# Kernel tuning notes

Hardware: AMD Instinct MI355X
Metric: run time of the kernel (lower is better)

The kernel has to match this reference:

```python
import jax, jax.numpy as jnp
import numpy as np

K = 3  # kernel_size
PAD = 1


def _unfold3x3(x):
    # x: [b, c, h, w] -> patches [b, c, k*k, h, w] matching torch.nn.Unfold
    # ordering (row-major over the kernel window, channel outermost).
    b, c, h, w = x.shape
    xp = jnp.pad(x, ((0, 0), (0, 0), (PAD, PAD), (PAD, PAD)))
    patches = jnp.stack(
        [xp[:, :, i:i + h, j:j + w] for i in range(K) for j in range(K)],
        axis=2,
    )
    return patches  # [b, c, 9, h, w]


def setup_inputs() -> dict:
    key = jax.random.key(0)
    k1, k2, k3, k4 = jax.random.split(key, 4)
    b, c, h, w = 8, 64, 128, 128
    out_ch = 64
    x = jax.random.normal(k1, (b, c, h, w), dtype=jnp.float32)
    guide_ch = jax.random.normal(k2, (b, c, h, w), dtype=jnp.float32)
    guide_sp = jax.random.normal(k3, (b, K * K, h, w), dtype=jnp.float32)
    # kaiming_normal_ fan_out on [out, in, k^2, 1, 1]: fan_out = out * k^2 * 1 * 1?
    # torch fan_out for 5D conv weight = out_channels * receptive_field (k^2*1*1)
    fan_out = out_ch * (K * K)
    std = np.sqrt(2.0 / fan_out)
    weight = jax.random.normal(k4, (out_ch, c, K * K), dtype=jnp.float32) * std
    return {"x": x, "guide_ch": guide_ch, "guide_sp": guide_sp, "weight": weight}


def reference(x, guide_ch, guide_sp, weight):
    # filter: [b, c, k^2, h, w] = 1 + tanh(guide_ch[:, :, None] + guide_sp[:, None])
    filt = 1.0 + jnp.tanh(guide_ch[:, :, None, :, :] + guide_sp[:, None, :, :, :])
    patches = _unfold3x3(x)  # [b, c, 9, h, w]
    # conv3d with weight [out, in, k^2, 1, 1] == per-pixel reduction over (c, k^2)
    out = jnp.einsum('bckhw,ock->bohw', patches * filt, weight)
    return out
```

## Files before the change

### kernel.cpp

```cpp
#include <hip/hip_runtime.h>
#include <hip/hip_bf16.h>

typedef short short8 __attribute__((ext_vector_type(8)));
typedef float floatx4 __attribute__((ext_vector_type(4)));
typedef unsigned uintx4 __attribute__((ext_vector_type(4)));

#define HWSZ 16384
#define WD 128
#define CD 64
#define OD 64
#define XSTR 72
#define OSTR 136
#define L2E2 2.8853900817779268f

__device__ __forceinline__ short f2bf(float f) {
    unsigned u = __builtin_bit_cast(unsigned, f);
    u += 0x7FFFu + ((u >> 16) & 1u);
    return (short)(u >> 16);
}

__device__ __forceinline__ unsigned pack2bf(float a, float b) {
    __hip_bfloat162 h = __float22bfloat162_rn(float2{a, b});
    unsigned u;
    __builtin_memcpy(&u, &h, 4);
    return u;
}

__device__ __forceinline__ float bf2f(short s) {
    return __builtin_bit_cast(float, ((unsigned)(unsigned short)s) << 16);
}

__global__ void prepack_w(const float* __restrict__ wgt, unsigned short* __restrict__ wp) {
    int idx = blockIdx.x * 256 + threadIdx.x;
    if (idx < 9 * 64 * 64) {
        int k = idx >> 12, o = (idx >> 6) & 63, c = idx & 63;
        wp[idx] = (unsigned short)f2bf(2.0f * wgt[o * 576 + c * 9 + k]);
    }
}

__global__ __launch_bounds__(256, 3)
void paka_kernel(const float* __restrict__ x, const float* __restrict__ gc,
                 const float* __restrict__ gs, const float* __restrict__ wgt,
                 const unsigned short* __restrict__ wp, float* __restrict__ out)
{
    __shared__ union {
        short xl[130 * XSTR];
        float o[64 * OSTR];
    } lds;

    const int tid  = threadIdx.x;
    const int wave = tid >> 6;
    const int lane = tid & 63;

    const int id  = blockIdx.x;
    const int swz = (id & 7) * 128 + (id >> 3);
    const int b = swz >> 7;
    const int h = swz & 127;

    const float* xb  = x  + (size_t)b * CD * HWSZ;
    const float* gcb = gc + (size_t)b * CD * HWSZ;
    const float* gsb = gs + (size_t)b * 9 * HWSZ;

    const int row = lane & 15;
    const int q   = lane >> 4;
    const int mt0 = wave * 2;

    float eg[2][2][8];
    #pragma unroll
    for (int mt = 0; mt < 2; ++mt) {
        int p = (mt0 + mt) * 16 + row;
        #pragma unroll
        for (int ks = 0; ks < 2; ++ks)
            #pragma unroll
            for (int j = 0; j < 8; ++j) {
                int c = ks * 32 + q * 8 + j;
                eg[mt][ks][j] = __builtin_amdgcn_exp2f(gcb[(size_t)c * HWSZ + h * WD + p] * L2E2);
            }
    }
    float esv[9][2];
    #pragma unroll
    for (int k = 0; k < 9; ++k)
        #pragma unroll
        for (int mt = 0; mt < 2; ++mt) {
            int p = (mt0 + mt) * 16 + row;
            esv[k][mt] = __builtin_amdgcn_exp2f(gsb[k * HWSZ + h * WD + p] * L2E2);
        }

    if (tid < 32)
        *(unsigned*)&lds.xl[0 * XSTR + tid * 2] = 0u;
    else if (tid < 64)
        *(unsigned*)&lds.xl[129 * XSTR + (tid - 32) * 2] = 0u;

    floatx4 acc[2][4];
    #pragma unroll
    for (int i = 0; i < 2; ++i)
        #pragma unroll
        for (int n = 0; n < 4; ++n)
            acc[i][n] = (floatx4){0.f, 0.f, 0.f, 0.f};

    #pragma unroll
    for (int dh = 0; dh < 3; ++dh) {
        const int hh = h + dh - 1;
        if ((unsigned)hh >= 128u) continue;

        __syncthreads();

        {
            const int g = tid >> 5;
            const float* xg = xb + (size_t)(8 * g) * HWSZ + hh * WD;
            #pragma unroll
            for (int it = 0; it < 4; ++it) {
                int p = it * 32 + (tid & 31);
                uintx4 pv;
                #pragma unroll
                for (int cc = 0; cc < 4; ++cc) {
                    float a  = xg[(size_t)(2 * cc) * HWSZ + p];
                    float b2 = xg[(size_t)(2 * cc + 1) * HWSZ + p];
                    pv[cc] = pack2bf(a, b2);
                }
                *(uintx4*)&lds.xl[(p + 1) * XSTR + g * 8] = pv;
            }
        }

        __syncthreads();

        #pragma unroll
        for (int dw = 0; dw < 3; ++dw) {
            const int k = dh * 3 + dw;
            #pragma unroll
            for (int ks = 0; ks < 2; ++ks) {
                short8 bv0, bv1, bv2, bv3;
                if (wp) {
                    const unsigned short* wk = wp + k * 4096 + ks * 32 + q * 8;
                    bv0 = *(const short8*)&wk[(0 * 16 + row) * 64];
                    bv1 = *(const short8*)&wk[(1 * 16 + row) * 64];
                    bv2 = *(const short8*)&wk[(2 * 16 + row) * 64];
                    bv3 = *(const short8*)&wk[(3 * 16 + row) * 64];
                } else {
                    #pragma unroll
                    for (int j = 0; j < 8; ++j) {
                        int c = ks * 32 + q * 8 + j;
                        bv0[j] = f2bf(2.0f * wgt[(0*16+row) * 576 + c * 9 + k]);
                        bv1[j] = f2bf(2.0f * wgt[(1*16+row) * 576 + c * 9 + k]);
                        bv2[j] = f2bf(2.0f * wgt[(2*16+row) * 576 + c * 9 + k]);
                        bv3[j] = f2bf(2.0f * wgt[(3*16+row) * 576 + c * 9 + k]);
                    }
                }

                short8 af[2];
                #pragma unroll
                for (int mt = 0; mt < 2; ++mt) {
                    int wslot = (mt0 + mt) * 16 + row + dw;
                    short8 raw = *(const short8*)&lds.xl[wslot * XSTR + ks * 32 + q * 8];
                    float es = esv[k][mt];
                    #pragma unroll
                    for (int jj = 0; jj < 4; ++jj) {
                        float d0 = fmaf(eg[mt][ks][2 * jj],     es, 1.0f);
                        float d1 = fmaf(eg[mt][ks][2 * jj + 1], es, 1.0f);
                        float r0 = __builtin_amdgcn_rcpf(d0);
                        float r1 = __builtin_amdgcn_rcpf(d1);
                        float x0 = bf2f(raw[2 * jj]);
                        float x1 = bf2f(raw[2 * jj + 1]);
                        float t0 = fmaf(-x0, r0, x0);
                        float t1 = fmaf(-x1, r1, x1);
                        ((unsigned*)&af[mt])[jj] = pack2bf(t0, t1);
                    }
                }
                acc[0][0] = __builtin_amdgcn_mfma_f32_16x16x32_bf16(af[0], bv0, acc[0][0], 0, 0, 0);
                acc[1][0] = __builtin_amdgcn_mfma_f32_16x16x32_bf16(af[1], bv0, acc[1][0], 0, 0, 0);
                acc[0][1] = __builtin_amdgcn_mfma_f32_16x16x32_bf16(af[0], bv1, acc[0][1], 0, 0, 0);
                acc[1][1] = __builtin_amdgcn_mfma_f32_16x16x32_bf16(af[1], bv1, acc[1][1], 0, 0, 0);
                acc[0][2] = __builtin_amdgcn_mfma_f32_16x16x32_bf16(af[0], bv2, acc[0][2], 0, 0, 0);
                acc[1][2] = __builtin_amdgcn_mfma_f32_16x16x32_bf16(af[1], bv2, acc[1][2], 0, 0, 0);
                acc[0][3] = __builtin_amdgcn_mfma_f32_16x16x32_bf16(af[0], bv3, acc[0][3], 0, 0, 0);
                acc[1][3] = __builtin_amdgcn_mfma_f32_16x16x32_bf16(af[1], bv3, acc[1][3], 0, 0, 0);
            }
        }
    }

    __syncthreads();

    #pragma unroll
    for (int i = 0; i < 2; ++i) {
        int prow = (mt0 + i) * 16 + q * 4;
        #pragma unroll
        for (int nt = 0; nt < 4; ++nt) {
            int o = nt * 16 + row;
            *(floatx4*)&lds.o[o * OSTR + prow] = acc[i][nt];
        }
    }

    __syncthreads();

    float* outb = out + ((size_t)b * OD) * HWSZ + h * WD;
    #pragma unroll
    for (int it = 0; it < 8; ++it) {
        int idx = it * 256 + tid;
        int o = idx >> 5, p4 = (idx & 31) * 4;
        *(floatx4*)&outb[(size_t)o * HWSZ + p4] = *(const floatx4*)&lds.o[o * OSTR + p4];
    }
}

extern "C" void kernel_launch(void* const* d_in, const int* in_sizes, int n_in,
                              void* d_out, int out_size, void* d_ws, size_t ws_size,
                              hipStream_t stream) {
    const float* x   = (const float*)d_in[0];
    const float* gcp = (const float*)d_in[1];
    const float* gsp = (const float*)d_in[2];
    const float* wgt = (const float*)d_in[3];
    float* out = (float*)d_out;

    const bool use_wp = ws_size >= (size_t)(9 * 64 * 64 * sizeof(unsigned short));
    unsigned short* wp = use_wp ? (unsigned short*)d_ws : nullptr;
    if (use_wp)
        prepack_w<<<dim3(144), dim3(256), 0, stream>>>(wgt, wp);
    paka_kernel<<<dim3(1024), dim3(256), 0, stream>>>(x, gcp, gsp, wgt, wp, out);
}
```

Baseline: 148.3 us.

## Stage all three input rows into LDS upfront with a single barrier

The kernel now loads all three halo rows of x into three LDS buffers at the start, before the exp computations, instead of reloading one row per dh iteration with two barriers each. This replaces six barriers with one and lets the global loads of all rows overlap each other and the guide loads. Out-of-range rows are zero-filled, so the border-row skip is gone and the boundary blocks do some extra MFMA work on zeros. LDS use roughly triples (about 56KB), so launch bounds drop from 3 to 2 blocks per CU, which lowers occupancy.

```diff
diff --git a/kernel.cpp b/kernel.cpp
--- a/kernel.cpp
+++ b/kernel.cpp
@@ -38,13 +38,13 @@
     }
 }
 
-__global__ __launch_bounds__(256, 3)
+__global__ __launch_bounds__(256, 2)
 void paka_kernel(const float* __restrict__ x, const float* __restrict__ gc,
                  const float* __restrict__ gs, const float* __restrict__ wgt,
                  const unsigned short* __restrict__ wp, float* __restrict__ out)
 {
     __shared__ union {
-        short xl[130 * XSTR];
+        short x3[3][130 * XSTR];
         float o[64 * OSTR];
     } lds;
 
@@ -64,6 +64,31 @@
     const int row = lane & 15;
     const int q   = lane >> 4;
     const int mt0 = wave * 2;
+    const int g   = tid >> 5;
+    const int pl  = tid & 31;
+
+    #pragma unroll
+    for (int r = 0; r < 3; ++r) {
+        const int hh = h + r - 1;
+        const bool ok = (unsigned)hh < 128u;
+        const float* xg = xb + (size_t)(8 * g) * HWSZ + (size_t)hh * WD;
+        #pragma unroll
+        for (int it = 0; it < 4; ++it) {
+            int p = it * 32 + pl;
+            uintx4 pv = (uintx4){0u, 0u, 0u, 0u};
+            if (ok) {
+                #pragma unroll
+                for (int cc = 0; cc < 4; ++cc)
+                    pv[cc] = pack2bf(xg[(size_t)(2 * cc) * HWSZ + p],
+                                     xg[(size_t)(2 * cc + 1) * HWSZ + p]);
+            }
+            *(uintx4*)&lds.x3[r][(p + 1) * XSTR + g * 8] = pv;
+        }
+    }
+    if (tid < 192) {
+        int r = tid >> 6, side = (tid >> 5) & 1, t = tid & 31;
+        *(unsigned*)&lds.x3[r][(side ? 129 : 0) * XSTR + t * 2] = 0u;
+    }
 
     float eg[2][2][8];
     #pragma unroll
@@ -86,11 +111,6 @@
             esv[k][mt] = __builtin_amdgcn_exp2f(gsb[k * HWSZ + h * WD + p] * L2E2);
         }
 
-    if (tid < 32)
-        *(unsigned*)&lds.xl[0 * XSTR + tid * 2] = 0u;
-    else if (tid < 64)
-        *(unsigned*)&lds.xl[129 * XSTR + (tid - 32) * 2] = 0u;
-
     floatx4 acc[2][4];
     #pragma unroll
     for (int i = 0; i < 2; ++i)
@@ -98,32 +118,11 @@
         for (int n = 0; n < 4; ++n)
             acc[i][n] = (floatx4){0.f, 0.f, 0.f, 0.f};
 
+    __syncthreads();
+
     #pragma unroll
     for (int dh = 0; dh < 3; ++dh) {
-        const int hh = h + dh - 1;
-        if ((unsigned)hh >= 128u) continue;
-
-        __syncthreads();
-
-        {
-            const int g = tid >> 5;
-            const float* xg = xb + (size_t)(8 * g) * HWSZ + hh * WD;
-            #pragma unroll
-            for (int it = 0; it < 4; ++it) {
-                int p = it * 32 + (tid & 31);
-                uintx4 pv;
-                #pragma unroll
-                for (int cc = 0; cc < 4; ++cc) {
-                    float a  = xg[(size_t)(2 * cc) * HWSZ + p];
-                    float b2 = xg[(size_t)(2 * cc + 1) * HWSZ + p];
-                    pv[cc] = pack2bf(a, b2);
-                }
-                *(uintx4*)&lds.xl[(p + 1) * XSTR + g * 8] = pv;
-            }
-        }
-
-        __syncthreads();
-
+        const short* cur = lds.x3[dh];
         #pragma unroll
         for (int dw = 0; dw < 3; ++dw) {
             const int k = dh * 3 + dw;
@@ -151,7 +150,7 @@
                 #pragma unroll
                 for (int mt = 0; mt < 2; ++mt) {
                     int wslot = (mt0 + mt) * 16 + row + dw;
-                    short8 raw = *(const short8*)&lds.xl[wslot * XSTR + ks * 32 + q * 8];
+                    short8 raw = *(const short8*)&cur[wslot * XSTR + ks * 32 + q * 8];
                     float es = esv[k][mt];
                     #pragma unroll
                     for (int jj = 0; jj < 4; ++jj) {
```

New measurement: 153.0 us. +3.2%, slower.

## Load x patches directly into registers instead of staging rows through LDS

Applied to the files above, without the earlier changes.

Removes the LDS staging of each input row and its two barriers per kernel row. Each lane now loads its own three horizontal neighbours for 32 channels straight from global memory, packs them to bf16 in registers, and zeroes out-of-range columns. The spatial guide exponentials are computed per kernel row rather than all up front, and launch bounds drop from 3 to 2 blocks per CU to leave room for more registers. The cost is roughly three times as many global x loads per block, with strided per-channel access instead of coalesced row loads, plus lower occupancy.

```diff
diff --git a/kernel.cpp b/kernel.cpp
--- a/kernel.cpp
+++ b/kernel.cpp
@@ -3,13 +3,11 @@
 
 typedef short short8 __attribute__((ext_vector_type(8)));
 typedef float floatx4 __attribute__((ext_vector_type(4)));
-typedef unsigned uintx4 __attribute__((ext_vector_type(4)));
 
 #define HWSZ 16384
 #define WD 128
 #define CD 64
 #define OD 64
-#define XSTR 72
 #define OSTR 136
 #define L2E2 2.8853900817779268f
 
@@ -38,15 +36,12 @@
     }
 }
 
-__global__ __launch_bounds__(256, 3)
+__global__ __launch_bounds__(256, 2)
 void paka_kernel(const float* __restrict__ x, const float* __restrict__ gc,
                  const float* __restrict__ gs, const float* __restrict__ wgt,
                  const unsigned short* __restrict__ wp, float* __restrict__ out)
 {
-    __shared__ union {
-        short xl[130 * XSTR];
-        float o[64 * OSTR];
-    } lds;
+    __shared__ float ldso[64 * OSTR];
 
     const int tid  = threadIdx.x;
     const int wave = tid >> 6;
@@ -77,19 +72,6 @@
                 eg[mt][ks][j] = __builtin_amdgcn_exp2f(gcb[(size_t)c * HWSZ + h * WD + p] * L2E2);
             }
     }
-    float esv[9][2];
-    #pragma unroll
-    for (int k = 0; k < 9; ++k)
-        #pragma unroll
-        for (int mt = 0; mt < 2; ++mt) {
-            int p = (mt0 + mt) * 16 + row;
-            esv[k][mt] = __builtin_amdgcn_exp2f(gsb[k * HWSZ + h * WD + p] * L2E2);
-        }
-
-    if (tid < 32)
-        *(unsigned*)&lds.xl[0 * XSTR + tid * 2] = 0u;
-    else if (tid < 64)
-        *(unsigned*)&lds.xl[129 * XSTR + (tid - 32) * 2] = 0u;
 
     floatx4 acc[2][4];
     #pragma unroll
@@ -103,82 +85,86 @@
         const int hh = h + dh - 1;
         if ((unsigned)hh >= 128u) continue;
 
-        __syncthreads();
-
-        {
-            const int g = tid >> 5;
-            const float* xg = xb + (size_t)(8 * g) * HWSZ + hh * WD;
-            #pragma unroll
-            for (int it = 0; it < 4; ++it) {
-                int p = it * 32 + (tid & 31);
-                uintx4 pv;
+        float es[3][2];
+        #pragma unroll
+        for (int dw = 0; dw < 3; ++dw)
+            #pragma unroll
+            for (int mt = 0; mt < 2; ++mt) {
+                int p = (mt0 + mt) * 16 + row;
+                es[dw][mt] = __builtin_amdgcn_exp2f(gsb[(dh * 3 + dw) * HWSZ + h * WD + p] * L2E2);
+            }
+
+        const float* xh = xb + (size_t)hh * WD;
+
+        #pragma unroll
+        for (int mt = 0; mt < 2; ++mt) {
+            const int pg = (mt0 + mt) * 16 + row;
+
+            unsigned xp[2][3][4];
+            #pragma unroll
+            for (int t = 0; t < 3; ++t) {
+                int w = pg + t - 1;
+                bool valid = (unsigned)w < 128u;
+                const float* xa = xh + (valid ? w : 0);
                 #pragma unroll
-                for (int cc = 0; cc < 4; ++cc) {
-                    float a  = xg[(size_t)(2 * cc) * HWSZ + p];
-                    float b2 = xg[(size_t)(2 * cc + 1) * HWSZ + p];
-                    pv[cc] = pack2bf(a, b2);
-                }
-                *(uintx4*)&lds.xl[(p + 1) * XSTR + g * 8] = pv;
-            }
-        }
-
-        __syncthreads();
-
-        #pragma unroll
-        for (int dw = 0; dw < 3; ++dw) {
-            const int k = dh * 3 + dw;
-            #pragma unroll
-            for (int ks = 0; ks < 2; ++ks) {
-                short8 bv0, bv1, bv2, bv3;
-                if (wp) {
-                    const unsigned short* wk = wp + k * 4096 + ks * 32 + q * 8;
-                    bv0 = *(const short8*)&wk[(0 * 16 + row) * 64];
-                    bv1 = *(const short8*)&wk[(1 * 16 + row) * 64];
-                    bv2 = *(const short8*)&wk[(2 * 16 + row) * 64];
-                    bv3 = *(const short8*)&wk[(3 * 16 + row) * 64];
-                } else {
+                for (int ks = 0; ks < 2; ++ks) {
+                    int c0 = ks * 32 + q * 8;
                     #pragma unroll
-                    for (int j = 0; j < 8; ++j) {
-                        int c = ks * 32 + q * 8 + j;
-                        bv0[j] = f2bf(2.0f * wgt[(0*16+row) * 576 + c * 9 + k]);
-                        bv1[j] = f2bf(2.0f * wgt[(1*16+row) * 576 + c * 9 + k]);
-                        bv2[j] = f2bf(2.0f * wgt[(2*16+row) * 576 + c * 9 + k]);
-                        bv3[j] = f2bf(2.0f * wgt[(3*16+row) * 576 + c * 9 + k]);
+                    for (int jj = 0; jj < 4; ++jj) {
+                        float a  = xa[(size_t)(c0 + 2 * jj)     * HWSZ];
+                        float b2 = xa[(size_t)(c0 + 2 * jj + 1) * HWSZ];
+                        unsigned pk = pack2bf(a, b2);
+                        xp[ks][t][jj] = valid ? pk : 0u;
                     }
                 }
-
-                short8 af[2];
+            }
+
+            #pragma unroll
+            for (int dw = 0; dw < 3; ++dw) {
+                const int k = dh * 3 + dw;
+                const float esk = es[dw][mt];
                 #pragma unroll
-                for (int mt = 0; mt < 2; ++mt) {
-                    int wslot = (mt0 + mt) * 16 + row + dw;
-                    short8 raw = *(const short8*)&lds.xl[wslot * XSTR + ks * 32 + q * 8];
-                    float es = esv[k][mt];
+                for (int ks = 0; ks < 2; ++ks) {
+                    short8 bv0, bv1, bv2, bv3;
+                    if (wp) {
+                        const unsigned short* wk = wp + k * 4096 + ks * 32 + q * 8;
+                        bv0 = *(const short8*)&wk[(0 * 16 + row) * 64];
+                        bv1 = *(const short8*)&wk[(1 * 16 + row) * 64];
+                        bv2 = *(const short8*)&wk[(2 * 16 + row) * 64];
+                        bv3 = *(const short8*)&wk[(3 * 16 + row) * 64];
+                    } else {
+                        #pragma unroll
+                        for (int j = 0; j < 8; ++j) {
+                            int c = ks * 32 + q * 8 + j;
+                            bv0[j] = f2bf(2.0f * wgt[(0*16+row) * 576 + c * 9 + k]);
+                            bv1[j] = f2bf(2.0f * wgt[(1*16+row) * 576 + c * 9 + k]);
+                            bv2[j] = f2bf(2.0f * wgt[(2*16+row) * 576 + c * 9 + k]);
+                            bv3[j] = f2bf(2.0f * wgt[(3*16+row) * 576 + c * 9 + k]);
+                        }
+                    }
+
+                    short8 af;
                     #pragma unroll
                     for (int jj = 0; jj < 4; ++jj) {
-                        float d0 = fmaf(eg[mt][ks][2 * jj],     es, 1.0f);
-                        float d1 = fmaf(eg[mt][ks][2 * jj + 1], es, 1.0f);
+                        float d0 = fmaf(eg[mt][ks][2 * jj],     esk, 1.0f);
+                        float d1 = fmaf(eg[mt][ks][2 * jj + 1], esk, 1.0f);
                         float r0 = __builtin_amdgcn_rcpf(d0);
                         float r1 = __builtin_amdgcn_rcpf(d1);
-                        float x0 = bf2f(raw[2 * jj]);
-                        float x1 = bf2f(raw[2 * jj + 1]);
+                        unsigned pk = xp[ks][dw][jj];
+                        float x0 = bf2f((short)(pk & 0xffffu));
+                        float x1 = bf2f((short)(pk >> 16));
                         float t0 = fmaf(-x0, r0, x0);
                         float t1 = fmaf(-x1, r1, x1);
-                        ((unsigned*)&af[mt])[jj] = pack2bf(t0, t1);
+                        ((unsigned*)&af)[jj] = pack2bf(t0, t1);
                     }
+                    acc[mt][0] = __builtin_amdgcn_mfma_f32_16x16x32_bf16(af, bv0, acc[mt][0], 0, 0, 0);
+                    acc[mt][1] = __builtin_amdgcn_mfma_f32_16x16x32_bf16(af, bv1, acc[mt][1], 0, 0, 0);
+                    acc[mt][2] = __builtin_amdgcn_mfma_f32_16x16x32_bf16(af, bv2, acc[mt][2], 0, 0, 0);
+                    acc[mt][3] = __builtin_amdgcn_mfma_f32_16x16x32_bf16(af, bv3, acc[mt][3], 0, 0, 0);
                 }
-                acc[0][0] = __builtin_amdgcn_mfma_f32_16x16x32_bf16(af[0], bv0, acc[0][0], 0, 0, 0);
-                acc[1][0] = __builtin_amdgcn_mfma_f32_16x16x32_bf16(af[1], bv0, acc[1][0], 0, 0, 0);
-                acc[0][1] = __builtin_amdgcn_mfma_f32_16x16x32_bf16(af[0], bv1, acc[0][1], 0, 0, 0);
-                acc[1][1] = __builtin_amdgcn_mfma_f32_16x16x32_bf16(af[1], bv1, acc[1][1], 0, 0, 0);
-                acc[0][2] = __builtin_amdgcn_mfma_f32_16x16x32_bf16(af[0], bv2, acc[0][2], 0, 0, 0);
-                acc[1][2] = __builtin_amdgcn_mfma_f32_16x16x32_bf16(af[1], bv2, acc[1][2], 0, 0, 0);
-                acc[0][3] = __builtin_amdgcn_mfma_f32_16x16x32_bf16(af[0], bv3, acc[0][3], 0, 0, 0);
-                acc[1][3] = __builtin_amdgcn_mfma_f32_16x16x32_bf16(af[1], bv3, acc[1][3], 0, 0, 0);
             }
         }
     }
-
-    __syncthreads();
 
     #pragma unroll
     for (int i = 0; i < 2; ++i) {
@@ -186,7 +172,7 @@
         #pragma unroll
         for (int nt = 0; nt < 4; ++nt) {
             int o = nt * 16 + row;
-            *(floatx4*)&lds.o[o * OSTR + prow] = acc[i][nt];
+            *(floatx4*)&ldso[o * OSTR + prow] = acc[i][nt];
         }
     }
 
@@ -197,7 +183,7 @@
     for (int it = 0; it < 8; ++it) {
         int idx = it * 256 + tid;
         int o = idx >> 5, p4 = (idx & 31) * 4;
-        *(floatx4*)&outb[(size_t)o * HWSZ + p4] = *(const floatx4*)&lds.o[o * OSTR + p4];
+        *(floatx4*)&outb[(size_t)o * HWSZ + p4] = *(const floatx4*)&ldso[o * OSTR + p4];
     }
 }
 
```

Measured after the change: 244.7 us. 1.65x slower.
